# Optimization experiments

Hardware: AMD Instinct MI355X
Metric: run time of the kernel (lower is better)

The kernel has to match this reference:

```python
import jax, jax.numpy as jnp
import numpy as np

C = 1024
H = C // 64          # 16 heads
CH = 64              # head dim
NUM_BUCKETS = 32
MAX_DISTANCE = 64
REL_SCALE = float(np.sqrt(CH))  # (channels//num_heads)**0.5 = 8
EPS = 1e-5


def group_norm(x, gamma, beta, groups):
    # x: [B, C, T]
    B, Cc, T = x.shape
    xg = x.reshape(B, groups, -1)
    m = xg.mean(-1, keepdims=True)
    v = xg.var(-1, keepdims=True)
    xn = ((xg - m) * jax.lax.rsqrt(v + EPS)).reshape(B, Cc, T)
    return xn * gamma[None, :, None] + beta[None, :, None]


def conv1d(x, w, b, pad):
    # x: [B, Cin, T], w: [Cout, Cin, K]
    y = jax.lax.conv_general_dilated(x, w, (1,), [(pad, pad)],
                                     dimension_numbers=('NCH', 'OIH', 'NCH'))
    return y + b[None, :, None]


def rel_pos_bias(T, emb):
    # lucidrains RelativePositionBias, non-causal; emb: [num_buckets, H]
    pos = jnp.arange(T)
    n = pos[:, None] - pos[None, :]          # n = -(k - q) = q - k
    half = NUM_BUCKETS // 2                  # 16
    ret = (n < 0).astype(jnp.int32) * half
    n = jnp.abs(n)
    max_exact = half // 2                    # 8
    is_small = n < max_exact
    nf = jnp.maximum(n, 1).astype(jnp.float32)
    val_large = max_exact + (jnp.log(nf / max_exact)
                             / np.log(MAX_DISTANCE / max_exact)
                             * (half - max_exact)).astype(jnp.int32)
    val_large = jnp.minimum(val_large, half - 1)
    bucket = ret + jnp.where(is_small, n, val_large)  # [T, T]
    return emb[bucket].transpose(2, 0, 1)             # [H, T, T]


def setup_inputs() -> dict:
    key = jax.random.key(0)
    ks = jax.random.split(key, 20)
    B, T = 8, 1024
    s = 0.02
    return {
        'x': jax.random.normal(ks[0], (B, C, T), jnp.float32),
        # ResBlock in_layers
        'rb_gn1_g': jnp.ones((C,), jnp.float32),
        'rb_gn1_b': jnp.zeros((C,), jnp.float32),
        'rb_conv1_w': jax.random.normal(ks[1], (C, C, 3), jnp.float32) * s,
        'rb_conv1_b': jnp.zeros((C,), jnp.float32),
        # ResBlock out_layers (zero-init in original; randomized for testing)
        'rb_gn2_g': jnp.ones((C,), jnp.float32),
        'rb_gn2_b': jnp.zeros((C,), jnp.float32),
        'rb_conv2_w': jax.random.normal(ks[2], (C, C, 3), jnp.float32) * s,
        'rb_conv2_b': jnp.zeros((C,), jnp.float32),
        # outer GroupNorm(8, C)
        'norm_g': jnp.ones((C,), jnp.float32),
        'norm_b': jnp.zeros((C,), jnp.float32),
        # AttentionBlock
        'attn_gn_g': jnp.ones((C,), jnp.float32),
        'attn_gn_b': jnp.zeros((C,), jnp.float32),
        'qkv_w': jax.random.normal(ks[3], (3 * C, C, 1), jnp.float32) * s,
        'qkv_b': jnp.zeros((3 * C,), jnp.float32),
        'proj_w': jax.random.normal(ks[4], (C, C, 1), jnp.float32) * s,
        'proj_b': jnp.zeros((C,), jnp.float32),
        'rel_emb': jax.random.normal(ks[5], (NUM_BUCKETS, H), jnp.float32) * s,
    }


def reference(x, rb_gn1_g, rb_gn1_b, rb_conv1_w, rb_conv1_b,
              rb_gn2_g, rb_gn2_b, rb_conv2_w, rb_conv2_b,
              norm_g, norm_b, attn_gn_g, attn_gn_b,
              qkv_w, qkv_b, proj_w, proj_b, rel_emb):
    B, Cc, T = x.shape
    # ResBlock: GN32 -> SiLU -> conv3 -> GN32 -> SiLU -> (dropout=0) -> conv3, + skip
    h = jax.nn.silu(group_norm(x, rb_gn1_g, rb_gn1_b, 32))
    h = conv1d(h, rb_conv1_w, rb_conv1_b, 1)
    h = jax.nn.silu(group_norm(h, rb_gn2_g, rb_gn2_b, 32))
    h = conv1d(h, rb_conv2_w, rb_conv2_b, 1)
    h = x + h
    # outer GroupNorm(8)
    h = group_norm(h, norm_g, norm_b, 8)
    # AttentionBlock with relative position bias
    xin = h
    qkv = conv1d(group_norm(h, attn_gn_g, attn_gn_b, 32), qkv_w, qkv_b, 0)
    # channel layout after reshape(bs*H, 3*ch, T): [H, 3, ch]
    qkv = qkv.reshape(B, H, 3, CH, T)
    q, k, v = qkv[:, :, 0], qkv[:, :, 1], qkv[:, :, 2]
    scale = CH ** -0.25
    w = jnp.einsum('bhct,bhcs->bhts', q * scale, k * scale)
    bias = rel_pos_bias(T, rel_emb) * REL_SCALE       # [H, T, T]
    w = jax.nn.softmax((w + bias[None]).astype(jnp.float32), axis=-1).astype(w.dtype)
    a = jnp.einsum('bhts,bhcs->bhct', w, v).reshape(B, Cc, T)
    return xin + conv1d(a, proj_w, proj_b, 0)
```

## Files before the change

### kernel.cpp

```cpp
#include <hip/hip_runtime.h>

typedef __attribute__((ext_vector_type(4))) float f32x4;
typedef __attribute__((ext_vector_type(8))) __bf16 bf16x8;
typedef __attribute__((ext_vector_type(4))) unsigned short us4;
typedef __attribute__((ext_vector_type(8))) unsigned short us8;

#define DEVI static __device__ __forceinline__

DEVI unsigned short f2bf(float f){
  union { float f; unsigned u; } x; x.f = f;
  unsigned r = x.u + 0x7fffu + ((x.u >> 16) & 1u);
  return (unsigned short)(r >> 16);
}
DEVI float bf2f(unsigned short h){
  union { unsigned u; float f; } x; x.u = ((unsigned)h) << 16;
  return x.f;
}

typedef __attribute__((address_space(1))) unsigned int gu32;
typedef __attribute__((address_space(3))) unsigned int lu32;
DEVI void gll16(const void* g, void* l){
  __builtin_amdgcn_global_load_lds((gu32*)g, (lu32*)l, 16, 0, 0);
}

DEVI f32x4 mfma16(bf16x8 a, bf16x8 b, f32x4 c){
  return __builtin_amdgcn_mfma_f32_16x16x32_bf16(a, b, c, 0, 0, 0);
}

DEVI float wredsum(float v){
  #pragma unroll
  for (int m = 1; m < 64; m <<= 1) v += __shfl_xor(v, m);
  return v;
}

__global__ __launch_bounds__(256) void conv_w_prep(const float* __restrict__ w,
                                                   unsigned short* __restrict__ wp){
  int idx = blockIdx.x * 256 + threadIdx.x;
  const float* p = w + (size_t)idx * 3;
  wp[idx]           = f2bf(p[0]);
  wp[1048576 + idx] = f2bf(p[1]);
  wp[2097152 + idx] = f2bf(p[2]);
}

__global__ __launch_bounds__(256) void cast_f2b(const float* __restrict__ in,
                                                unsigned short* __restrict__ out, int n4){
  int idx = blockIdx.x * 256 + threadIdx.x;
  if (idx < n4){
    f32x4 v = *(const f32x4*)&in[(size_t)idx * 4];
    us4 o;
    #pragma unroll
    for (int j = 0; j < 4; j++) o[j] = f2bf(v[j]);
    *(us4*)&out[(size_t)idx * 4] = o;
  }
}

__global__ __launch_bounds__(256) void btab_k(const float* __restrict__ emb,
                                              float* __restrict__ btab){
  int idx = blockIdx.x * 256 + threadIdx.x;
  if (idx >= 2047 * 16) return;
  int d = idx >> 4, h = idx & 15;
  int n0 = d - 1023;
  int ret = (n0 < 0) ? 16 : 0;
  int n = (n0 < 0) ? -n0 : n0;
  int bucket;
  if (n < 8) bucket = ret + n;
  else {
    float ratio = logf((float)n * 0.125f) / 2.0794415416798357f;
    int vl = 8 + (int)(ratio * 8.0f);
    bucket = ret + (vl < 15 ? vl : 15);
  }
  btab[h * 2048 + d] = emb[bucket * 16 + h] * 11.541560327111707f;
}

__global__ __launch_bounds__(256) void zero_pads(unsigned short* __restrict__ h1p,
                                                 unsigned short* __restrict__ g2p){
  int idx = blockIdx.x * 256 + threadIdx.x;
  int b = idx >> 11, rr = (idx >> 10) & 1, c = idx & 1023;
  size_t off = ((size_t)b * 1026 + (rr ? 1025 : 0)) * 1024 + c;
  h1p[off] = 0; g2p[off] = 0;
}

__global__ __launch_bounds__(256) void gn_stats_cast(const float* __restrict__ in,
                                                     float2* __restrict__ st,
                                                     unsigned short* __restrict__ xb){
  const int g = blockIdx.x; const int tid = threadIdx.x;
  const float* p = in + (size_t)g * 32768;
  unsigned short* q = xb + (size_t)g * 32768;
  float s = 0.f, s2 = 0.f;
  for (int i = tid * 4; i < 32768; i += 1024){
    f32x4 v = *(const f32x4*)&p[i];
    us4 o;
    #pragma unroll
    for (int j = 0; j < 4; j++){ s += v[j]; s2 += v[j] * v[j]; o[j] = f2bf(v[j]); }
    *(us4*)&q[i] = o;
  }
  s = wredsum(s); s2 = wredsum(s2);
  __shared__ float rs[4], rs2[4];
  if ((tid & 63) == 0){ rs[tid >> 6] = s; rs2[tid >> 6] = s2; }
  __syncthreads();
  if (tid == 0){
    float S = rs[0] + rs[1] + rs[2] + rs[3];
    float S2 = rs2[0] + rs2[1] + rs2[2] + rs2[3];
    float m = S * (1.f / 32768.f);
    float var = S2 * (1.f / 32768.f) - m * m;
    st[g] = make_float2(m, rsqrtf(var + 1e-5f));
  }
}

__global__ __launch_bounds__(256) void gn_stats_bf16(const unsigned short* __restrict__ in,
                                                     float2* __restrict__ st){
  const int g = blockIdx.x; const int tid = threadIdx.x;
  const unsigned short* p = in + (size_t)g * 32768;
  float s = 0.f, s2 = 0.f;
  for (int i = tid * 8; i < 32768; i += 2048){
    us8 v = *(const us8*)&p[i];
    #pragma unroll
    for (int j = 0; j < 8; j++){ float f = bf2f(v[j]); s += f; s2 += f * f; }
  }
  s = wredsum(s); s2 = wredsum(s2);
  __shared__ float rs[4], rs2[4];
  if ((tid & 63) == 0){ rs[tid >> 6] = s; rs2[tid >> 6] = s2; }
  __syncthreads();
  if (tid == 0){
    float S = rs[0] + rs[1] + rs[2] + rs[3];
    float S2 = rs2[0] + rs2[1] + rs2[2] + rs2[3];
    float m = S * (1.f / 32768.f);
    float var = S2 * (1.f / 32768.f) - m * m;
    st[g] = make_float2(m, rsqrtf(var + 1e-5f));
  }
}

template<int SILU, int INBF16, int OUTPAD>
__global__ __launch_bounds__(256) void gn_apply_tr(
    const void* __restrict__ inp, const float2* __restrict__ st,
    const float* __restrict__ gma, const float* __restrict__ bta,
    unsigned short* __restrict__ out)
{
  const int gid = blockIdx.x;
  const int tc = gid & 15, g = (gid >> 4) & 31, b = gid >> 9;
  const int tid = threadIdx.x;
  const int t0 = tc * 64;
  __shared__ __align__(16) unsigned short tr[64 * 40];
  float2 s = st[b * 32 + g];
  int c = tid >> 3, t8 = (tid & 7) * 8;
  int ch = g * 32 + c;
  float sc = gma[ch] * s.y;
  float sh = bta[ch] - s.x * sc;
  float vv[8];
  if (INBF16){
    const unsigned short* p = (const unsigned short*)inp + ((size_t)b * 1024 + ch) * 1024 + t0 + t8;
    us8 v = *(const us8*)p;
    #pragma unroll
    for (int j = 0; j < 8; j++) vv[j] = bf2f(v[j]);
  } else {
    const float* p = (const float*)inp + ((size_t)b * 1024 + ch) * 1024 + t0 + t8;
    f32x4 v0 = *(const f32x4*)p; f32x4 v1 = *(const f32x4*)(p + 4);
    #pragma unroll
    for (int j = 0; j < 4; j++){ vv[j] = v0[j]; vv[4 + j] = v1[j]; }
  }
  #pragma unroll
  for (int j = 0; j < 8; j++){
    float v = vv[j] * sc + sh;
    if (SILU) v = v / (1.f + __expf(-v));
    tr[(t8 + j) * 40 + c] = f2bf(v);
  }
  __syncthreads();
  int t = tid >> 2, c8 = (tid & 3) * 8;
  us8 d = *(const us8*)&tr[t * 40 + c8];
  size_t row = OUTPAD ? ((size_t)b * 1026 + 1 + t0 + t) : ((size_t)b * 1024 + t0 + t);
  *(us8*)&out[row * 1024 + g * 32 + c8] = d;
}

__global__ __launch_bounds__(256) void gn2_partial(const unsigned short* __restrict__ c1,
                                                   float2* __restrict__ part){
  const int tid = threadIdx.x;
  const int ck = blockIdx.x & 31, b = blockIdx.x >> 5;
  const unsigned short* p = c1 + ((size_t)b * 1024 + ck * 32) * 1024 + tid * 4;
  float s = 0.f, s2 = 0.f;
  for (int r = 0; r < 32; r++){
    us4 v = *(const us4*)&p[(size_t)r * 1024];
    #pragma unroll
    for (int j = 0; j < 4; j++){ float f = bf2f(v[j]); s += f; s2 += f * f; }
  }
  __shared__ float ls[256], ls2[256];
  ls[tid] = s; ls2[tid] = s2;
  __syncthreads();
  if (tid < 32){
    float S = 0.f, S2 = 0.f;
    #pragma unroll
    for (int k = 0; k < 8; k++){ S += ls[tid * 8 + k]; S2 += ls2[tid * 8 + k]; }
    part[((size_t)b * 32 + ck) * 32 + tid] = make_float2(S, S2);
  }
}

template<int SILU>
__global__ __launch_bounds__(256) void gn2_apply(const unsigned short* __restrict__ c1,
    const float2* __restrict__ part, const float* __restrict__ gma, const float* __restrict__ bta,
    unsigned short* __restrict__ outp)
{
  const int tid = threadIdx.x;
  const int ck = blockIdx.x & 31, b = blockIdx.x >> 5;
  __shared__ float2 st[32];
  if (tid < 32){
    float S = 0.f, S2 = 0.f;
    for (int k = 0; k < 32; k++){ float2 pp = part[((size_t)b * 32 + k) * 32 + tid]; S += pp.x; S2 += pp.y; }
    float m = S * (1.f / 32768.f);
    float var = S2 * (1.f / 32768.f) - m * m;
    st[tid] = make_float2(m, rsqrtf(var + 1e-5f));
  }
  __syncthreads();
  float2 s = st[tid >> 3];
  float sc[4], sh[4];
  #pragma unroll
  for (int j = 0; j < 4; j++){ int ch = tid * 4 + j; sc[j] = gma[ch] * s.y; sh[j] = bta[ch] - s.x * sc[j]; }
  const unsigned short* p = c1 + ((size_t)b * 1024 + ck * 32) * 1024 + tid * 4;
  unsigned short* q = outp + ((size_t)b * 1026 + 1 + ck * 32) * 1024 + tid * 4;
  for (int r = 0; r < 32; r++){
    us4 v = *(const us4*)&p[(size_t)r * 1024];
    us4 o;
    #pragma unroll
    for (int j = 0; j < 4; j++){
      float f = bf2f(v[j]) * sc[j] + sh[j];
      if (SILU) f = f / (1.f + __expf(-f));
      o[j] = f2bf(f);
    }
    *(us4*)&q[(size_t)r * 1024] = o;
  }
}

__global__ __launch_bounds__(256) void gn8_partial(const unsigned short* __restrict__ r,
                                                   float2* __restrict__ part){
  const int gid = blockIdx.x; const int tid = threadIdx.x;
  const int sub = gid & 15, g = (gid >> 4) & 7, b = gid >> 7;
  const unsigned short* p = r + ((size_t)(b * 8 + g)) * 131072 + sub * 8192;
  float s = 0.f, s2 = 0.f;
  for (int i = tid * 8; i < 8192; i += 2048){
    us8 v = *(const us8*)&p[i];
    #pragma unroll
    for (int j = 0; j < 8; j++){ float f = bf2f(v[j]); s += f; s2 += f * f; }
  }
  s = wredsum(s); s2 = wredsum(s2);
  __shared__ float rs[4], rs2[4];
  if ((tid & 63) == 0){ rs[tid >> 6] = s; rs2[tid >> 6] = s2; }
  __syncthreads();
  if (tid == 0) part[gid] = make_float2(rs[0] + rs[1] + rs[2] + rs[3],
                                        rs2[0] + rs2[1] + rs2[2] + rs2[3]);
}

__global__ __launch_bounds__(256) void gn8_apply(const unsigned short* __restrict__ r,
    const float2* __restrict__ part, const float* __restrict__ gma, const float* __restrict__ bta,
    unsigned short* __restrict__ xin){
  const int gid = blockIdx.x; const int tid = threadIdx.x;
  const int sub = gid & 15, g = (gid >> 4) & 7, b = gid >> 7;
  __shared__ float2 stt;
  if (tid == 0){
    float S = 0.f, S2 = 0.f;
    #pragma unroll
    for (int k = 0; k < 16; k++){ float2 pp = part[(gid & ~15) + k]; S += pp.x; S2 += pp.y; }
    float m = S * (1.f / 131072.f);
    float var = S2 * (1.f / 131072.f) - m * m;
    stt = make_float2(m, rsqrtf(var + 1e-5f));
  }
  __syncthreads();
  float2 s = stt;
  const unsigned short* pr = r + ((size_t)(b * 8 + g)) * 131072 + sub * 8192;
  unsigned short* px = xin + ((size_t)(b * 8 + g)) * 131072 + sub * 8192;
  for (int i = tid * 8; i < 8192; i += 2048){
    int c = g * 128 + sub * 8 + (i >> 10);
    float sc = gma[c] * s.y, sh = bta[c] - s.x * sc;
    us8 v = *(const us8*)&pr[i];
    us8 o;
    #pragma unroll
    for (int j = 0; j < 8; j++) o[j] = f2bf(bf2f(v[j]) * sc + sh);
    *(us8*)&px[i] = o;
  }
}

template<int KK, int EPI>
__global__ __launch_bounds__(256, 2) void gemm_k(
    const unsigned short* __restrict__ inT,
    const unsigned short* __restrict__ W,
    const float* __restrict__ bias,
    void* __restrict__ outp,
    void* __restrict__ resp,
    int OC, int NT)
{
  __shared__ __align__(16) unsigned short Alds[2][128 * 64];
  __shared__ __align__(16) unsigned short Blds[2][128 * 64];
  const int tid = threadIdx.x;
  const int lane = tid & 63;
  const int w = tid >> 6;
  const int wn = w >> 1, wo = w & 1;
  const int nt = blockIdx.x % NT;
  const int ot = blockIdx.x / NT;
  const int b = nt >> 3;
  const int t0 = (nt & 7) * 128;
  const int ob = ot * 128;
  const int rowbase = (KK == 3) ? (b * 1026 + t0) : (b * 1024 + t0);
  const int NTI = KK * 16;

  f32x4 acc[4][4];
  #pragma unroll
  for (int m = 0; m < 4; m++)
    #pragma unroll
    for (int n = 0; n < 4; n++) acc[m][n] = 0.f;

  const int lrow = lane >> 3;
  const int lblk = lane & 7;

  auto stage = [&](int kt, int bufsel){
    int kk = kt >> 4;
    int i0 = (kt & 15) * 64;
    const unsigned short* Ab = inT + (size_t)(rowbase + kk) * 1024;
    const unsigned short* Bb = W + ((size_t)kk * OC + ob) * 1024;
    #pragma unroll
    for (int j = 0; j < 4; ++j){
      int chunk = w * 4 + j;
      int row = chunk * 8 + lrow;
      int gcol = (lblk ^ (row & 7)) * 8;
      gll16(Ab + (size_t)row * 1024 + i0 + gcol, &Alds[bufsel][chunk * 512]);
      gll16(Bb + (size_t)row * 1024 + i0 + gcol, &Blds[bufsel][chunk * 512]);
    }
  };

  stage(0, 0);
  stage(1, 1);
  asm volatile("s_waitcnt vmcnt(8)" ::: "memory");
  __builtin_amdgcn_sched_barrier(0);
  __builtin_amdgcn_s_barrier();
  __builtin_amdgcn_sched_barrier(0);

  #pragma unroll 2
  for (int kt = 0; kt < NTI; ++kt){
    const int cur = kt & 1;
    const unsigned short* Ab = &Alds[cur][0];
    const unsigned short* Bb = &Blds[cur][0];
    bf16x8 af[2][4], bfv[2][4];
    #pragma unroll
    for (int m = 0; m < 4; m++){
      int row = wn * 64 + m * 16 + (lane & 15);
      #pragma unroll
      for (int k2 = 0; k2 < 2; k2++){
        int blk = ((lane >> 4) + k2 * 4) ^ (row & 7);
        af[k2][m] = *(const bf16x8*)&Ab[row * 64 + blk * 8];
      }
    }
    #pragma unroll
    for (int n = 0; n < 4; n++){
      int row = wo * 64 + n * 16 + (lane & 15);
      #pragma unroll
      for (int k2 = 0; k2 < 2; k2++){
        int blk = ((lane >> 4) + k2 * 4) ^ (row & 7);
        bfv[k2][n] = *(const bf16x8*)&Bb[row * 64 + blk * 8];
      }
    }
    asm volatile("s_waitcnt lgkmcnt(0)" ::: "memory");
    __builtin_amdgcn_sched_barrier(0);
    __builtin_amdgcn_s_barrier();
    __builtin_amdgcn_sched_barrier(0);
    if (kt + 2 < NTI) stage(kt + 2, cur);
    __builtin_amdgcn_sched_barrier(0);
    __builtin_amdgcn_s_setprio(1);
    #pragma unroll
    for (int k2 = 0; k2 < 2; k2++)
      #pragma unroll
      for (int m = 0; m < 4; m++)
        #pragma unroll
        for (int n = 0; n < 4; n++)
          acc[m][n] = mfma16(af[k2][m], bfv[k2][n], acc[m][n]);
    __builtin_amdgcn_s_setprio(0);
    __builtin_amdgcn_sched_barrier(0);
    if (kt + 2 < NTI){ asm volatile("s_waitcnt vmcnt(8)" ::: "memory"); }
    else             { asm volatile("s_waitcnt vmcnt(0)" ::: "memory"); }
    __builtin_amdgcn_sched_barrier(0);
    __builtin_amdgcn_s_barrier();
    __builtin_amdgcn_sched_barrier(0);
  }

  if (EPI == 0){
    unsigned short* out = (unsigned short*)outp;
    #pragma unroll
    for (int m = 0; m < 4; m++){
      int tl = t0 + wn * 64 + m * 16 + ((lane >> 4) * 4);
      #pragma unroll
      for (int n = 0; n < 4; n++){
        int o = ob + wo * 64 + n * 16 + (lane & 15);
        float bz = bias[o];
        size_t base = ((size_t)b * 1024 + tl) * OC + o;
        #pragma unroll
        for (int r = 0; r < 4; r++)
          out[base + (size_t)r * OC] = f2bf(acc[m][n][r] + bz);
      }
    }
  } else if (EPI == 3){
    unsigned short* qkT = (unsigned short*)outp;
    unsigned short* vT  = (unsigned short*)resp;
    #pragma unroll
    for (int m = 0; m < 4; m++){
      int tl = t0 + wn * 64 + m * 16 + ((lane >> 4) * 4);
      #pragma unroll
      for (int n = 0; n < 4; n++){
        int o0 = ob + wo * 64 + n * 16;
        int h = o0 / 192;
        int rem0 = o0 - h * 192;
        int o = o0 + (lane & 15);
        float bz = bias[o];
        if (rem0 < 128){
          size_t base = ((size_t)b * 1024 + tl) * 2048 + h * 128 + rem0 + (lane & 15);
          #pragma unroll
          for (int r = 0; r < 4; r++)
            qkT[base + (size_t)r * 2048] = f2bf(acc[m][n][r] + bz);
        } else {
          int c = rem0 - 128 + (lane & 15);
          size_t base = (((size_t)(b * 16 + h)) * 64 + c) * 1024 + tl;
          us4 o4;
          #pragma unroll
          for (int r = 0; r < 4; r++) o4[r] = f2bf(acc[m][n][r] + bz);
          *(us4*)&vT[base] = o4;
        }
      }
    }
  } else if (EPI == 4){
    unsigned short* out = (unsigned short*)outp;
    const unsigned short* xr = (const unsigned short*)resp;
    #pragma unroll
    for (int m = 0; m < 4; m++){
      int tl = t0 + wn * 64 + m * 16 + ((lane >> 4) * 4);
      #pragma unroll
      for (int n = 0; n < 4; n++){
        int o = ob + wo * 64 + n * 16 + (lane & 15);
        float bz = bias[o];
        size_t base = ((size_t)b * 1024 + o) * 1024 + tl;
        us4 xv = *(const us4*)&xr[base];
        us4 ov;
        #pragma unroll
        for (int r = 0; r < 4; r++) ov[r] = f2bf(bf2f(xv[r]) + acc[m][n][r] + bz);
        *(us4*)&out[base] = ov;
      }
    }
  } else {
    float* out = (float*)outp;
    #pragma unroll
    for (int m = 0; m < 4; m++){
      int tl = t0 + wn * 64 + m * 16 + ((lane >> 4) * 4);
      #pragma unroll
      for (int n = 0; n < 4; n++){
        int o = ob + wo * 64 + n * 16 + (lane & 15);
        float bz = bias[o];
        size_t base = ((size_t)b * 1024 + o) * 1024 + tl;
        const unsigned short* xr = (const unsigned short*)resp;
        us4 xv = *(const us4*)&xr[base];
        f32x4 v;
        v[0] = bf2f(xv[0]); v[1] = bf2f(xv[1]); v[2] = bf2f(xv[2]); v[3] = bf2f(xv[3]);
        #pragma unroll
        for (int r = 0; r < 4; r++) v[r] += acc[m][n][r] + bz;
        *(f32x4*)&out[base] = v;
      }
    }
  }
}

__global__ __launch_bounds__(256, 2) void attn_k6(
    const unsigned short* __restrict__ qkT,
    const unsigned short* __restrict__ vT,
    const float* __restrict__ btab,
    unsigned short* __restrict__ aT)
{
  __shared__ __align__(16) unsigned short Kb[2][64 * 64];
  __shared__ __align__(16) unsigned short Vb[2][64 * 64];
  __shared__ __align__(16) unsigned short Pb[4][32 * 64];
  __shared__ __align__(16) unsigned short blds[1152];
  const int tid = threadIdx.x, lane = tid & 63, w = tid >> 6;
  const int d0 = blockIdx.x;
  const int xcd = d0 & 7, slot = d0 >> 3;
  const int bh = xcd * 16 + (slot >> 3);
  const int qt = slot & 7;
  const int h = bh & 15, b = bh >> 4;
  const int q0b = qt * 128;
  const int q0 = q0b + w * 32;
  const unsigned short* qk = qkT + (size_t)b * 1024 * 2048 + h * 128;
  const unsigned short* vh = vT + ((size_t)(b * 16 + h)) * 64 * 1024;
  const int lc = lane & 15, lg = lane >> 4;

  const float bneg = btab[h * 2048 + 0];
  const float bpos = btab[h * 2048 + 2046];

  for (int i = tid; i < 1151; i += 256)
    blds[i] = f2bf(btab[h * 2048 + q0b + i]);

  bf16x8 qf[2][2];
  #pragma unroll
  for (int m = 0; m < 2; m++){
    const unsigned short* qrow = qk + (size_t)(q0 + m * 16 + lc) * 2048;
    #pragma unroll
    for (int k2 = 0; k2 < 2; k2++)
      qf[m][k2] = *(const bf16x8*)&qrow[k2 * 32 + lg * 8];
  }
  float m_run[2], l_run[2];
  f32x4 oacc[2][4];
  m_run[0] = m_run[1] = -1e30f; l_run[0] = l_run[1] = 0.f;
  #pragma unroll
  for (int m = 0; m < 2; m++)
    #pragma unroll
    for (int cb = 0; cb < 4; cb++) oacc[m][cb] = 0.f;

  const int lr = lane >> 3, lb = lane & 7;
  const float qs = 0.18033688011112042f;

  #pragma unroll
  for (int j = 0; j < 2; j++){
    int chunk = w * 2 + j;
    int row = chunk * 8 + lr;
    int gcol = (lb ^ (row & 7)) * 8;
    gll16(qk + 64 + (size_t)row * 2048 + gcol, &Kb[0][chunk * 512]);
    gll16(vh + (size_t)row * 1024 + gcol, &Vb[0][chunk * 512]);
  }
  __syncthreads();

  for (int t = 0; t < 16; ++t){
    const int cur = t & 1;
    const int st0 = t * 64;
    if (t < 15){
      int nst = st0 + 64;
      #pragma unroll
      for (int j = 0; j < 2; j++){
        int chunk = w * 2 + j;
        int row = chunk * 8 + lr;
        int gcol = (lb ^ (row & 7)) * 8;
        gll16(qk + 64 + (size_t)(nst + row) * 2048 + gcol, &Kb[cur ^ 1][chunk * 512]);
        gll16(vh + (size_t)row * 1024 + nst + gcol, &Vb[cur ^ 1][chunk * 512]);
      }
    }
    f32x4 sfr[2][4];
    #pragma unroll
    for (int m = 0; m < 2; m++)
      #pragma unroll
      for (int sub = 0; sub < 4; sub++) sfr[m][sub] = 0.f;
    __builtin_amdgcn_s_setprio(1);
    #pragma unroll
    for (int sub = 0; sub < 4; sub++){
      int row = sub * 16 + lc;
      #pragma unroll
      for (int k2 = 0; k2 < 2; k2++){
        int blk = (lg + k2 * 4) ^ (row & 7);
        bf16x8 bk = *(const bf16x8*)&Kb[cur][row * 64 + blk * 8];
        sfr[0][sub] = mfma16(bk, qf[0][k2], sfr[0][sub]);
        sfr[1][sub] = mfma16(bk, qf[1][k2], sfr[1][sub]);
      }
    }
    __builtin_amdgcn_s_setprio(0);
    const bool unineg = (st0 >= q0 + 81);
    const bool unipos = (st0 + 113 <= q0);
    const bool uni = unineg || unipos;
    const float bc = unineg ? bneg : bpos;
    float pm2[2];
    if (uni){
      #pragma unroll
      for (int m = 0; m < 2; m++){
        float x0 = fmaxf(fmaxf(sfr[m][0][0], sfr[m][0][1]), fmaxf(sfr[m][0][2], sfr[m][0][3]));
        float x1 = fmaxf(fmaxf(sfr[m][1][0], sfr[m][1][1]), fmaxf(sfr[m][1][2], sfr[m][1][3]));
        float x2 = fmaxf(fmaxf(sfr[m][2][0], sfr[m][2][1]), fmaxf(sfr[m][2][2], sfr[m][2][3]));
        float x3 = fmaxf(fmaxf(sfr[m][3][0], sfr[m][3][1]), fmaxf(sfr[m][3][2], sfr[m][3][3]));
        float pm = fmaxf(fmaxf(x0, x1), fmaxf(x2, x3)) * qs + bc;
        pm = fmaxf(pm, __shfl_xor(pm, 16));
        pm = fmaxf(pm, __shfl_xor(pm, 32));
        pm2[m] = pm;
      }
    } else {
      #pragma unroll
      for (int m = 0; m < 2; m++){
        const unsigned short* bp = &blds[(w * 32 + m * 16 + lc) + 960 - st0];
        #pragma unroll
        for (int sub = 0; sub < 4; sub++){
          int off = 63 - sub * 16 - lg * 4;
          #pragma unroll
          for (int r = 0; r < 4; r++)
            sfr[m][sub][r] = sfr[m][sub][r] * qs + bf2f(bp[off - r]);
        }
        float x0 = fmaxf(fmaxf(sfr[m][0][0], sfr[m][0][1]), fmaxf(sfr[m][0][2], sfr[m][0][3]));
        float x1 = fmaxf(fmaxf(sfr[m][1][0], sfr[m][1][1]), fmaxf(sfr[m][1][2], sfr[m][1][3]));
        float x2 = fmaxf(fmaxf(sfr[m][2][0], sfr[m][2][1]), fmaxf(sfr[m][2][2], sfr[m][2][3]));
        float x3 = fmaxf(fmaxf(sfr[m][3][0], sfr[m][3][1]), fmaxf(sfr[m][3][2], sfr[m][3][3]));
        float pm = fmaxf(fmaxf(x0, x1), fmaxf(x2, x3));
        pm = fmaxf(pm, __shfl_xor(pm, 16));
        pm = fmaxf(pm, __shfl_xor(pm, 32));
        pm2[m] = pm;
      }
    }
    const bool stable = (pm2[0] <= m_run[0] + 8.f) && (pm2[1] <= m_run[1] + 8.f);
    const bool resc = !__all(stable);
    float corr[2], mref[2];
    if (resc){
      #pragma unroll
      for (int m = 0; m < 2; m++){
        float mn = fmaxf(m_run[m], pm2[m]);
        corr[m] = exp2f(m_run[m] - mn);
        m_run[m] = mn; mref[m] = mn;
      }
    } else { mref[0] = m_run[0]; mref[1] = m_run[1]; }
    const float scl = uni ? qs : 1.f;
    #pragma unroll
    for (int m = 0; m < 2; m++){
      const float ad = (uni ? bc : 0.f) - mref[m];
      float ssum = 0.f;
      #pragma unroll
      for (int sub = 0; sub < 4; sub++)
        #pragma unroll
        for (int r = 0; r < 4; r++){
          float e = exp2f(fmaf(sfr[m][sub][r], scl, ad));
          sfr[m][sub][r] = e;
          ssum += e;
        }
      ssum += __shfl_xor(ssum, 16);
      ssum += __shfl_xor(ssum, 32);
      l_run[m] = resc ? (l_run[m] * corr[m] + ssum) : (l_run[m] + ssum);
    }
    if (resc){
      #pragma unroll
      for (int m = 0; m < 2; m++)
        #pragma unroll
        for (int r = 0; r < 4; r++){
          float co = __shfl(corr[m], lg * 4 + r);
          #pragma unroll
          for (int cb = 0; cb < 4; cb++) oacc[m][cb][r] *= co;
        }
    }
    unsigned short* P = &Pb[w][0];
    #pragma unroll
    for (int m = 0; m < 2; m++){
      int qrow = m * 16 + lc;
      int rsw = (qrow & 7) << 3;
      #pragma unroll
      for (int sub = 0; sub < 4; sub++){
        int col = sub * 16 + lg * 4;
        unsigned w0, w1;
        asm("v_cvt_pk_bf16_f32 %0, %1, %2" : "=v"(w0) : "v"(sfr[m][sub][0]), "v"(sfr[m][sub][1]));
        asm("v_cvt_pk_bf16_f32 %0, %1, %2" : "=v"(w1) : "v"(sfr[m][sub][2]), "v"(sfr[m][sub][3]));
        uint2 pk; pk.x = w0; pk.y = w1;
        *(uint2*)&P[qrow * 64 + (col ^ rsw)] = pk;
      }
    }
    __builtin_amdgcn_s_setprio(1);
    #pragma unroll
    for (int k2 = 0; k2 < 2; k2++){
      bf16x8 pa[2];
      #pragma unroll
      for (int m = 0; m < 2; m++){
        int rowp = m * 16 + lc;
        int blkp = (lg + k2 * 4) ^ (rowp & 7);
        pa[m] = *(const bf16x8*)&P[rowp * 64 + blkp * 8];
      }
      #pragma unroll
      for (int cb = 0; cb < 4; cb++){
        int ch = cb * 16 + lc;
        int blkv = (lg + k2 * 4) ^ (ch & 7);
        bf16x8 bv = *(const bf16x8*)&Vb[cur][ch * 64 + blkv * 8];
        oacc[0][cb] = mfma16(pa[0], bv, oacc[0][cb]);
        oacc[1][cb] = mfma16(pa[1], bv, oacc[1][cb]);
      }
    }
    __builtin_amdgcn_s_setprio(0);
    __syncthreads();
  }
  #pragma unroll
  for (int m = 0; m < 2; m++)
    #pragma unroll
    for (int r = 0; r < 4; r++){
      float li = 1.0f / __shfl(l_run[m], lg * 4 + r);
      int tq = q0 + m * 16 + lg * 4 + r;
      #pragma unroll
      for (int cb = 0; cb < 4; cb++){
        int ch = h * 64 + cb * 16 + lc;
        aT[((size_t)b * 1024 + tq) * 1024 + ch] = f2bf(oacc[m][cb][r] * li);
      }
    }
}

extern "C" void kernel_launch(void* const* d_in, const int* in_sizes, int n_in,
                              void* d_out, int out_size, void* d_ws, size_t ws_size,
                              hipStream_t stream)
{
  const float* x       = (const float*)d_in[0];
  const float* gn1_g   = (const float*)d_in[1];
  const float* gn1_b   = (const float*)d_in[2];
  const float* conv1_w = (const float*)d_in[3];
  const float* conv1_b = (const float*)d_in[4];
  const float* gn2_g   = (const float*)d_in[5];
  const float* gn2_b   = (const float*)d_in[6];
  const float* conv2_w = (const float*)d_in[7];
  const float* conv2_b = (const float*)d_in[8];
  const float* norm_g  = (const float*)d_in[9];
  const float* norm_b  = (const float*)d_in[10];
  const float* agn_g   = (const float*)d_in[11];
  const float* agn_b   = (const float*)d_in[12];
  const float* qkv_w   = (const float*)d_in[13];
  const float* qkv_b   = (const float*)d_in[14];
  const float* proj_w  = (const float*)d_in[15];
  const float* proj_b  = (const float*)d_in[16];
  const float* rel_emb = (const float*)d_in[17];

  if (ws_size < 139526144u) return;

  char* ws = (char*)d_ws;
  unsigned short* w1p   = (unsigned short*)(ws + 0);
  unsigned short* w2p   = (unsigned short*)(ws + 6291456);
  unsigned short* wqkv  = (unsigned short*)(ws + 12582912);
  unsigned short* wproj = (unsigned short*)(ws + 18874368);
  float* btab           = (float*)(ws + 20971520);
  float2* stats1        = (float2*)(ws + 21102592);
  float2* part2         = (float2*)(ws + 21104640);
  float2* stats32       = (float2*)(ws + 21170176);
  float2* part8         = (float2*)(ws + 21172224);
  unsigned short* h1p   = (unsigned short*)(ws + 22020096);
  unsigned short* c1    = (unsigned short*)(ws + 38830080);
  unsigned short* g2p   = (unsigned short*)(ws + 55607296);
  unsigned short* qkT   = h1p;
  unsigned short* vT    = (unsigned short*)(ws + 55574528);
  unsigned short* xb    = (unsigned short*)(ws + 72417280);
  unsigned short* attn_in = (unsigned short*)(ws + 72417280);
  unsigned short* xin   = (unsigned short*)(ws + 105971712);
  unsigned short* aT    = (unsigned short*)(ws + 122748928);

  conv_w_prep<<<4096, 256, 0, stream>>>(conv1_w, w1p);
  conv_w_prep<<<4096, 256, 0, stream>>>(conv2_w, w2p);
  cast_f2b<<<3072, 256, 0, stream>>>(qkv_w, wqkv, 3072 * 1024 / 4);
  cast_f2b<<<1024, 256, 0, stream>>>(proj_w, wproj, 1024 * 1024 / 4);
  btab_k<<<128, 256, 0, stream>>>(rel_emb, btab);
  zero_pads<<<64, 256, 0, stream>>>(h1p, g2p);

  gn_stats_cast<<<256, 256, 0, stream>>>(x, stats1, xb);
  gn_apply_tr<1, 0, 1><<<4096, 256, 0, stream>>>(x, stats1, gn1_g, gn1_b, h1p);

  gemm_k<3, 0><<<512, 256, 0, stream>>>(h1p, w1p, conv1_b, c1, nullptr, 1024, 64);

  gn2_partial<<<256, 256, 0, stream>>>(c1, part2);
  gn2_apply<1><<<256, 256, 0, stream>>>(c1, part2, gn2_g, gn2_b, g2p);

  gemm_k<3, 4><<<512, 256, 0, stream>>>(g2p, w2p, conv2_b, xb, xb, 1024, 64);

  gn8_partial<<<1024, 256, 0, stream>>>(xb, part8);
  gn8_apply<<<1024, 256, 0, stream>>>(xb, part8, norm_g, norm_b, xin);

  gn_stats_bf16<<<256, 256, 0, stream>>>(xin, stats32);
  gn_apply_tr<0, 1, 0><<<4096, 256, 0, stream>>>(xin, stats32, agn_g, agn_b, attn_in);

  gemm_k<1, 3><<<1536, 256, 0, stream>>>(attn_in, wqkv, qkv_b, qkT, vT, 3072, 64);

  attn_k6<<<1024, 256, 0, stream>>>(qkT, vT, btab, aT);

  gemm_k<1, 2><<<512, 256, 0, stream>>>(aT, wproj, proj_b, d_out, xin, 1024, 64);
}
```

Before: 372.6 us.

## Fuse group-norm statistics into GEMM epilogues and gn8 apply pass

GroupNorm partial sums are now computed in the conv GEMM epilogues and in the gn8 apply pass, replacing the separate stats kernels that re-read the activations. Tiny single-block finalize kernels turn the partials into mean and rstd. The first GN apply now reads the bf16 copy of x instead of fp32, and the attention bias table is kept in fp32 in LDS. This removes several full activation reads at the cost of heavier GEMM epilogues, extra syncs, and more LDS in attention.

```diff
diff --git a/kernel.cpp b/kernel.cpp
--- a/kernel.cpp
+++ b/kernel.cpp
@@ -107,27 +107,36 @@
   }
 }
 
-__global__ __launch_bounds__(256) void gn_stats_bf16(const unsigned short* __restrict__ in,
-                                                     float2* __restrict__ st){
-  const int g = blockIdx.x; const int tid = threadIdx.x;
-  const unsigned short* p = in + (size_t)g * 32768;
-  float s = 0.f, s2 = 0.f;
-  for (int i = tid * 8; i < 32768; i += 2048){
-    us8 v = *(const us8*)&p[i];
-    #pragma unroll
-    for (int j = 0; j < 8; j++){ float f = bf2f(v[j]); s += f; s2 += f * f; }
-  }
-  s = wredsum(s); s2 = wredsum(s2);
-  __shared__ float rs[4], rs2[4];
-  if ((tid & 63) == 0){ rs[tid >> 6] = s; rs2[tid >> 6] = s2; }
-  __syncthreads();
-  if (tid == 0){
-    float S = rs[0] + rs[1] + rs[2] + rs[3];
-    float S2 = rs2[0] + rs2[1] + rs2[2] + rs2[3];
-    float m = S * (1.f / 32768.f);
-    float var = S2 * (1.f / 32768.f) - m * m;
-    st[g] = make_float2(m, rsqrtf(var + 1e-5f));
-  }
+__global__ __launch_bounds__(256) void fin2_k(const float2* __restrict__ p, float2* __restrict__ st){
+  int idx = threadIdx.x;
+  int b = idx >> 5, ck = idx & 31;
+  float S = 0.f, S2 = 0.f;
+  #pragma unroll
+  for (int tt = 0; tt < 8; tt++){ float2 v = p[(size_t)(b * 8 + tt) * 32 + ck]; S += v.x; S2 += v.y; }
+  float m = S * (1.f / 32768.f);
+  float var = S2 * (1.f / 32768.f) - m * m;
+  st[idx] = make_float2(m, rsqrtf(var + 1e-5f));
+}
+__global__ __launch_bounds__(64) void fin8_k(const float2* __restrict__ p, float2* __restrict__ st){
+  int idx = threadIdx.x;
+  int b = idx >> 3, g = idx & 7;
+  float S = 0.f, S2 = 0.f;
+  #pragma unroll
+  for (int tt = 0; tt < 8; tt++){ float2 v = p[(size_t)(b * 8 + tt) * 8 + g]; S += v.x; S2 += v.y; }
+  float m = S * (1.f / 131072.f);
+  float var = S2 * (1.f / 131072.f) - m * m;
+  st[idx] = make_float2(m, rsqrtf(var + 1e-5f));
+}
+__global__ __launch_bounds__(256) void fin32_k(const float2* __restrict__ p, float2* __restrict__ st){
+  int idx = threadIdx.x;
+  int b = idx >> 5, gg = idx & 31;
+  int g8 = gg >> 2, k = gg & 3;
+  float S = 0.f, S2 = 0.f;
+  #pragma unroll
+  for (int j = 0; j < 4; j++){ float2 v = p[(size_t)(b * 8 + g8) * 16 + k * 4 + j]; S += v.x; S2 += v.y; }
+  float m = S * (1.f / 32768.f);
+  float var = S2 * (1.f / 32768.f) - m * m;
+  st[idx] = make_float2(m, rsqrtf(var + 1e-5f));
 }
 
 template<int SILU, int INBF16, int OUTPAD>
@@ -171,45 +180,14 @@
   *(us8*)&out[row * 1024 + g * 32 + c8] = d;
 }
 
-__global__ __launch_bounds__(256) void gn2_partial(const unsigned short* __restrict__ c1,
-                                                   float2* __restrict__ part){
-  const int tid = threadIdx.x;
-  const int ck = blockIdx.x & 31, b = blockIdx.x >> 5;
-  const unsigned short* p = c1 + ((size_t)b * 1024 + ck * 32) * 1024 + tid * 4;
-  float s = 0.f, s2 = 0.f;
-  for (int r = 0; r < 32; r++){
-    us4 v = *(const us4*)&p[(size_t)r * 1024];
-    #pragma unroll
-    for (int j = 0; j < 4; j++){ float f = bf2f(v[j]); s += f; s2 += f * f; }
-  }
-  __shared__ float ls[256], ls2[256];
-  ls[tid] = s; ls2[tid] = s2;
-  __syncthreads();
-  if (tid < 32){
-    float S = 0.f, S2 = 0.f;
-    #pragma unroll
-    for (int k = 0; k < 8; k++){ S += ls[tid * 8 + k]; S2 += ls2[tid * 8 + k]; }
-    part[((size_t)b * 32 + ck) * 32 + tid] = make_float2(S, S2);
-  }
-}
-
 template<int SILU>
 __global__ __launch_bounds__(256) void gn2_apply(const unsigned short* __restrict__ c1,
-    const float2* __restrict__ part, const float* __restrict__ gma, const float* __restrict__ bta,
+    const float2* __restrict__ st2f, const float* __restrict__ gma, const float* __restrict__ bta,
     unsigned short* __restrict__ outp)
 {
   const int tid = threadIdx.x;
   const int ck = blockIdx.x & 31, b = blockIdx.x >> 5;
-  __shared__ float2 st[32];
-  if (tid < 32){
-    float S = 0.f, S2 = 0.f;
-    for (int k = 0; k < 32; k++){ float2 pp = part[((size_t)b * 32 + k) * 32 + tid]; S += pp.x; S2 += pp.y; }
-    float m = S * (1.f / 32768.f);
-    float var = S2 * (1.f / 32768.f) - m * m;
-    st[tid] = make_float2(m, rsqrtf(var + 1e-5f));
-  }
-  __syncthreads();
-  float2 s = st[tid >> 3];
+  float2 s = st2f[b * 32 + (tid >> 3)];
   float sc[4], sh[4];
   #pragma unroll
   for (int j = 0; j < 4; j++){ int ch = tid * 4 + j; sc[j] = gma[ch] * s.y; sh[j] = bta[ch] - s.x * sc[j]; }
@@ -228,65 +206,50 @@
   }
 }
 
-__global__ __launch_bounds__(256) void gn8_partial(const unsigned short* __restrict__ r,
-                                                   float2* __restrict__ part){
+__global__ __launch_bounds__(256) void gn8_apply(const unsigned short* __restrict__ r,
+    const float2* __restrict__ st8f, const float* __restrict__ gma, const float* __restrict__ bta,
+    unsigned short* __restrict__ xin, float2* __restrict__ part32){
   const int gid = blockIdx.x; const int tid = threadIdx.x;
   const int sub = gid & 15, g = (gid >> 4) & 7, b = gid >> 7;
-  const unsigned short* p = r + ((size_t)(b * 8 + g)) * 131072 + sub * 8192;
-  float s = 0.f, s2 = 0.f;
-  for (int i = tid * 8; i < 8192; i += 2048){
-    us8 v = *(const us8*)&p[i];
-    #pragma unroll
-    for (int j = 0; j < 8; j++){ float f = bf2f(v[j]); s += f; s2 += f * f; }
-  }
-  s = wredsum(s); s2 = wredsum(s2);
-  __shared__ float rs[4], rs2[4];
-  if ((tid & 63) == 0){ rs[tid >> 6] = s; rs2[tid >> 6] = s2; }
-  __syncthreads();
-  if (tid == 0) part[gid] = make_float2(rs[0] + rs[1] + rs[2] + rs[3],
-                                        rs2[0] + rs2[1] + rs2[2] + rs2[3]);
-}
-
-__global__ __launch_bounds__(256) void gn8_apply(const unsigned short* __restrict__ r,
-    const float2* __restrict__ part, const float* __restrict__ gma, const float* __restrict__ bta,
-    unsigned short* __restrict__ xin){
-  const int gid = blockIdx.x; const int tid = threadIdx.x;
-  const int sub = gid & 15, g = (gid >> 4) & 7, b = gid >> 7;
-  __shared__ float2 stt;
-  if (tid == 0){
-    float S = 0.f, S2 = 0.f;
-    #pragma unroll
-    for (int k = 0; k < 16; k++){ float2 pp = part[(gid & ~15) + k]; S += pp.x; S2 += pp.y; }
-    float m = S * (1.f / 131072.f);
-    float var = S2 * (1.f / 131072.f) - m * m;
-    stt = make_float2(m, rsqrtf(var + 1e-5f));
-  }
-  __syncthreads();
-  float2 s = stt;
+  float2 s = st8f[b * 8 + g];
   const unsigned short* pr = r + ((size_t)(b * 8 + g)) * 131072 + sub * 8192;
   unsigned short* px = xin + ((size_t)(b * 8 + g)) * 131072 + sub * 8192;
+  float ps = 0.f, ps2 = 0.f;
   for (int i = tid * 8; i < 8192; i += 2048){
     int c = g * 128 + sub * 8 + (i >> 10);
     float sc = gma[c] * s.y, sh = bta[c] - s.x * sc;
     us8 v = *(const us8*)&pr[i];
     us8 o;
     #pragma unroll
-    for (int j = 0; j < 8; j++) o[j] = f2bf(bf2f(v[j]) * sc + sh);
+    for (int j = 0; j < 8; j++){
+      float f = bf2f(v[j]) * sc + sh;
+      ps += f; ps2 += f * f;
+      o[j] = f2bf(f);
+    }
     *(us8*)&px[i] = o;
   }
-}
-
-template<int KK, int EPI>
+  ps = wredsum(ps); ps2 = wredsum(ps2);
+  __shared__ float rs[4], rs2[4];
+  if ((tid & 63) == 0){ rs[tid >> 6] = ps; rs2[tid >> 6] = ps2; }
+  __syncthreads();
+  if (tid == 0)
+    part32[(size_t)(b * 8 + g) * 16 + sub] =
+      make_float2(rs[0] + rs[1] + rs[2] + rs[3], rs2[0] + rs2[1] + rs2[2] + rs2[3]);
+}
+
+template<int KK, int EPI, int GPART>
 __global__ __launch_bounds__(256, 2) void gemm_k(
     const unsigned short* __restrict__ inT,
     const unsigned short* __restrict__ W,
     const float* __restrict__ bias,
     void* __restrict__ outp,
     void* __restrict__ resp,
+    float2* __restrict__ part,
     int OC, int NT)
 {
   __shared__ __align__(16) unsigned short Alds[2][128 * 64];
   __shared__ __align__(16) unsigned short Blds[2][128 * 64];
+  __shared__ float sred[16];
   const int tid = threadIdx.x;
   const int lane = tid & 63;
   const int w = tid >> 6;
@@ -379,6 +342,7 @@
 
   if (EPI == 0){
     unsigned short* out = (unsigned short*)outp;
+    float ps[2] = {0.f, 0.f}, ps2[2] = {0.f, 0.f};
     #pragma unroll
     for (int m = 0; m < 4; m++){
       int tl = t0 + wn * 64 + m * 16 + ((lane >> 4) * 4);
@@ -388,8 +352,26 @@
         float bz = bias[o];
         size_t base = ((size_t)b * 1024 + tl) * OC + o;
         #pragma unroll
-        for (int r = 0; r < 4; r++)
-          out[base + (size_t)r * OC] = f2bf(acc[m][n][r] + bz);
+        for (int r = 0; r < 4; r++){
+          float v = acc[m][n][r] + bz;
+          if (GPART == 2){ ps[n >> 1] += v; ps2[n >> 1] += v * v; }
+          out[base + (size_t)r * OC] = f2bf(v);
+        }
+      }
+    }
+    if (GPART == 2){
+      #pragma unroll
+      for (int j = 0; j < 2; j++){ ps[j] = wredsum(ps[j]); ps2[j] = wredsum(ps2[j]); }
+      if (lane == 0){
+        sred[w * 4 + 0] = ps[0]; sred[w * 4 + 1] = ps2[0];
+        sred[w * 4 + 2] = ps[1]; sred[w * 4 + 3] = ps2[1];
+      }
+      __syncthreads();
+      if (tid < 4){
+        int g = tid, woo = g >> 1, jj = g & 1;
+        float S  = sred[woo * 4 + jj * 2 + 0] + sred[(woo + 2) * 4 + jj * 2 + 0];
+        float S2 = sred[woo * 4 + jj * 2 + 1] + sred[(woo + 2) * 4 + jj * 2 + 1];
+        part[(size_t)(b * 8 + (nt & 7)) * 32 + ot * 4 + g] = make_float2(S, S2);
       }
     }
   } else if (EPI == 3){
@@ -423,6 +405,7 @@
   } else if (EPI == 4){
     unsigned short* out = (unsigned short*)outp;
     const unsigned short* xr = (const unsigned short*)resp;
+    float ps = 0.f, ps2 = 0.f;
     #pragma unroll
     for (int m = 0; m < 4; m++){
       int tl = t0 + wn * 64 + m * 16 + ((lane >> 4) * 4);
@@ -434,8 +417,22 @@
         us4 xv = *(const us4*)&xr[base];
         us4 ov;
         #pragma unroll
-        for (int r = 0; r < 4; r++) ov[r] = f2bf(bf2f(xv[r]) + acc[m][n][r] + bz);
+        for (int r = 0; r < 4; r++){
+          float v = bf2f(xv[r]) + acc[m][n][r] + bz;
+          if (GPART == 8){ ps += v; ps2 += v * v; }
+          ov[r] = f2bf(v);
+        }
         *(us4*)&out[base] = ov;
+      }
+    }
+    if (GPART == 8){
+      ps = wredsum(ps); ps2 = wredsum(ps2);
+      if (lane == 0){ sred[w * 2] = ps; sred[w * 2 + 1] = ps2; }
+      __syncthreads();
+      if (tid == 0){
+        float S = sred[0] + sred[2] + sred[4] + sred[6];
+        float S2 = sred[1] + sred[3] + sred[5] + sred[7];
+        part[(size_t)(b * 8 + (nt & 7)) * 8 + ot] = make_float2(S, S2);
       }
     }
   } else {
@@ -460,7 +457,7 @@
   }
 }
 
-__global__ __launch_bounds__(256, 2) void attn_k6(
+__global__ __launch_bounds__(256, 2) void attn_k5(
     const unsigned short* __restrict__ qkT,
     const unsigned short* __restrict__ vT,
     const float* __restrict__ btab,
@@ -469,7 +466,7 @@
   __shared__ __align__(16) unsigned short Kb[2][64 * 64];
   __shared__ __align__(16) unsigned short Vb[2][64 * 64];
   __shared__ __align__(16) unsigned short Pb[4][32 * 64];
-  __shared__ __align__(16) unsigned short blds[1152];
+  __shared__ __align__(16) float blds[1152];
   const int tid = threadIdx.x, lane = tid & 63, w = tid >> 6;
   const int d0 = blockIdx.x;
   const int xcd = d0 & 7, slot = d0 >> 3;
@@ -486,7 +483,7 @@
   const float bpos = btab[h * 2048 + 2046];
 
   for (int i = tid; i < 1151; i += 256)
-    blds[i] = f2bf(btab[h * 2048 + q0b + i]);
+    blds[i] = btab[h * 2048 + q0b + i];
 
   bf16x8 qf[2][2];
   #pragma unroll
@@ -569,13 +566,13 @@
     } else {
       #pragma unroll
       for (int m = 0; m < 2; m++){
-        const unsigned short* bp = &blds[(w * 32 + m * 16 + lc) + 960 - st0];
+        const float* bp = &blds[(w * 32 + m * 16 + lc) + 960 - st0];
         #pragma unroll
         for (int sub = 0; sub < 4; sub++){
           int off = 63 - sub * 16 - lg * 4;
           #pragma unroll
           for (int r = 0; r < 4; r++)
-            sfr[m][sub][r] = sfr[m][sub][r] * qs + bf2f(bp[off - r]);
+            sfr[m][sub][r] = sfr[m][sub][r] * qs + bp[off - r];
         }
         float x0 = fmaxf(fmaxf(sfr[m][0][0], sfr[m][0][1]), fmaxf(sfr[m][0][2], sfr[m][0][3]));
         float x1 = fmaxf(fmaxf(sfr[m][1][0], sfr[m][1][1]), fmaxf(sfr[m][1][2], sfr[m][1][3]));
@@ -708,9 +705,12 @@
   unsigned short* wproj = (unsigned short*)(ws + 18874368);
   float* btab           = (float*)(ws + 20971520);
   float2* stats1        = (float2*)(ws + 21102592);
-  float2* part2         = (float2*)(ws + 21104640);
-  float2* stats32       = (float2*)(ws + 21170176);
-  float2* part8         = (float2*)(ws + 21172224);
+  float2* st2f          = (float2*)(ws + 21104640);
+  float2* st8f          = (float2*)(ws + 21106688);
+  float2* st32f         = (float2*)(ws + 21108736);
+  float2* part2n        = (float2*)(ws + 21110784);
+  float2* part8n        = (float2*)(ws + 21127168);
+  float2* part32        = (float2*)(ws + 21131264);
   unsigned short* h1p   = (unsigned short*)(ws + 22020096);
   unsigned short* c1    = (unsigned short*)(ws + 38830080);
   unsigned short* g2p   = (unsigned short*)(ws + 55607296);
@@ -729,24 +729,22 @@
   zero_pads<<<64, 256, 0, stream>>>(h1p, g2p);
 
   gn_stats_cast<<<256, 256, 0, stream>>>(x, stats1, xb);
-  gn_apply_tr<1, 0, 1><<<4096, 256, 0, stream>>>(x, stats1, gn1_g, gn1_b, h1p);
-
-  gemm_k<3, 0><<<512, 256, 0, stream>>>(h1p, w1p, conv1_b, c1, nullptr, 1024, 64);
-
-  gn2_partial<<<256, 256, 0, stream>>>(c1, part2);
-  gn2_apply<1><<<256, 256, 0, stream>>>(c1, part2, gn2_g, gn2_b, g2p);
-
-  gemm_k<3, 4><<<512, 256, 0, stream>>>(g2p, w2p, conv2_b, xb, xb, 1024, 64);
-
-  gn8_partial<<<1024, 256, 0, stream>>>(xb, part8);
-  gn8_apply<<<1024, 256, 0, stream>>>(xb, part8, norm_g, norm_b, xin);
-
-  gn_stats_bf16<<<256, 256, 0, stream>>>(xin, stats32);
-  gn_apply_tr<0, 1, 0><<<4096, 256, 0, stream>>>(xin, stats32, agn_g, agn_b, attn_in);
-
-  gemm_k<1, 3><<<1536, 256, 0, stream>>>(attn_in, wqkv, qkv_b, qkT, vT, 3072, 64);
-
-  attn_k6<<<1024, 256, 0, stream>>>(qkT, vT, btab, aT);
-
-  gemm_k<1, 2><<<512, 256, 0, stream>>>(aT, wproj, proj_b, d_out, xin, 1024, 64);
-}
+  gn_apply_tr<1, 1, 1><<<4096, 256, 0, stream>>>(xb, stats1, gn1_g, gn1_b, h1p);
+
+  gemm_k<3, 0, 2><<<512, 256, 0, stream>>>(h1p, w1p, conv1_b, c1, nullptr, part2n, 1024, 64);
+  fin2_k<<<1, 256, 0, stream>>>(part2n, st2f);
+  gn2_apply<1><<<256, 256, 0, stream>>>(c1, st2f, gn2_g, gn2_b, g2p);
+
+  gemm_k<3, 4, 8><<<512, 256, 0, stream>>>(g2p, w2p, conv2_b, xb, xb, part8n, 1024, 64);
+  fin8_k<<<1, 64, 0, stream>>>(part8n, st8f);
+  gn8_apply<<<1024, 256, 0, stream>>>(xb, st8f, norm_g, norm_b, xin, part32);
+  fin32_k<<<1, 256, 0, stream>>>(part32, st32f);
+
+  gn_apply_tr<0, 1, 0><<<4096, 256, 0, stream>>>(xin, st32f, agn_g, agn_b, attn_in);
+
+  gemm_k<1, 3, 0><<<1536, 256, 0, stream>>>(attn_in, wqkv, qkv_b, qkT, vT, nullptr, 3072, 64);
+
+  attn_k5<<<1024, 256, 0, stream>>>(qkT, vT, btab, aT);
+
+  gemm_k<1, 2, 0><<<512, 256, 0, stream>>>(aT, wproj, proj_b, d_out, xin, nullptr, 1024, 64);
+}
```

Result: faster. 361.3 us (-3.0%).
